# Performance work log

Measured on AMD Instinct MI355X. Metric: run time of the kernel, lower is better.

Reference implementation:

```python
import jax, jax.numpy as jnp
import numpy as np

N_GENE = 100000
N_DIS = 20000
H = 128
E = 500000


def setup_inputs() -> dict:
    key = jax.random.key(0)
    ks = jax.random.split(key, 12)
    s1 = 1.0 / np.sqrt(2 * H)  # fan-in init scale, Linear(2H, H)
    s2 = 1.0 / np.sqrt(H)      # fan-in init scale, Linear(H, 1)
    z_gene = jax.random.normal(ks[0], (N_GENE, H), jnp.float32)
    z_disease = jax.random.normal(ks[1], (N_DIS, H), jnp.float32)
    # gene->disease edges: row indexes genes, col indexes diseases
    edges_gd = jnp.stack([
        jax.random.randint(ks[2], (E,), 0, N_GENE),
        jax.random.randint(ks[3], (E,), 0, N_DIS),
    ])
    # gene->gene edges
    edges_gg = jnp.stack([
        jax.random.randint(ks[4], (E,), 0, N_GENE),
        jax.random.randint(ks[5], (E,), 0, N_GENE),
    ])
    return {
        "z_gene": z_gene,
        "z_disease": z_disease,
        "edges_gd": edges_gd,
        "edges_gg": edges_gg,
        "w1_gd": jax.random.normal(ks[6], (2 * H, H), jnp.float32) * s1,
        "b1_gd": jnp.zeros((H,), jnp.float32),
        "w2_gd": jax.random.normal(ks[7], (H, 1), jnp.float32) * s2,
        "b2_gd": jnp.zeros((1,), jnp.float32),
        "w1_gg": jax.random.normal(ks[8], (2 * H, H), jnp.float32) * s1,
        "b1_gg": jnp.zeros((H,), jnp.float32),
        "w2_gg": jax.random.normal(ks[9], (H, 1), jnp.float32) * s2,
        "b2_gg": jnp.zeros((1,), jnp.float32),
    }


def _decode(z_src, z_dst, edges, w1, b1, w2, b2):
    # gather src/dst node embeddings by edge index, concat -> [E, 2H]
    z = jnp.concatenate([z_src[edges[0]], z_dst[edges[1]]], axis=1)
    h = jnp.maximum(z @ w1 + b1, 0.0)  # Linear + ReLU
    return h @ w2 + b2                  # Linear -> [E, 1]


def reference(z_gene, z_disease, edges_gd, edges_gg,
              w1_gd, b1_gd, w2_gd, b2_gd,
              w1_gg, b1_gg, w2_gg, b2_gg):
    out_gd = _decode(z_gene, z_disease, edges_gd, w1_gd, b1_gd, w2_gd, b2_gd)
    out_gg = _decode(z_gene, z_gene, edges_gg, w1_gg, b1_gg, w2_gg, b2_gg)
    # dict of per-relation outputs in the original; stack since E matches
    return jnp.stack([out_gd, out_gg])  # [2, E, 1]
```

## Files before the change

kernel.cpp:

```cpp
#include <hip/hip_runtime.h>
#include <hip/hip_bf16.h>

#define HDIM 128

typedef __attribute__((ext_vector_type(8))) short short8;
typedef __attribute__((ext_vector_type(4))) float floatx4;

__device__ __forceinline__ float bf2f(unsigned short u) {
    return __uint_as_float(((unsigned)u) << 16);
}
__device__ __forceinline__ unsigned short f2b(float f) {
    __hip_bfloat16 h = __float2bfloat16(f);
    return __builtin_bit_cast(unsigned short, h);
}
__device__ __forceinline__ float ldv(const void* p, size_t i, int flag) {
    return flag ? bf2f(((const unsigned short*)p)[i]) : ((const float*)p)[i];
}
__device__ __forceinline__ short8 pack8(float4 a, float4 b) {
    short8 r;
    r[0] = (short)f2b(a.x); r[1] = (short)f2b(a.y);
    r[2] = (short)f2b(a.z); r[3] = (short)f2b(a.w);
    r[4] = (short)f2b(b.x); r[5] = (short)f2b(b.y);
    r[6] = (short)f2b(b.z); r[7] = (short)f2b(b.w);
    return r;
}

__device__ __forceinline__ int local_detect(const unsigned short* zbits) {
    __shared__ int red[256];
    int tid = threadIdx.x;
    int cnt = 0;
    for (int i = tid; i < 4096; i += 256) {
        int ex = (zbits[i] >> 7) & 0xFF;
        if (ex >= 100 && ex <= 140) cnt++;
    }
    red[tid] = cnt;
    __syncthreads();
    for (int s = 128; s > 0; s >>= 1) {
        if (tid < s) red[tid] += red[tid + s];
        __syncthreads();
    }
    return (red[0] >= 3686) ? 1 : 0;
}

__global__ __launch_bounds__(256) void prep_kernel(
    const unsigned short* __restrict__ zbits,
    const void* __restrict__ w1_gd, const void* __restrict__ w1_gg,
    const void* __restrict__ b1_gd, const void* __restrict__ w2_gd,
    const void* __restrict__ b2_gd, const void* __restrict__ b1_gg,
    const void* __restrict__ w2_gg, const void* __restrict__ b2_gg,
    unsigned short* __restrict__ img, float* __restrict__ params,
    int* __restrict__ flagout)
{
    int flag = local_detect(zbits);
    int b = blockIdx.x;
    int tid = threadIdx.x;
    if (b < 32) {
        int im   = b >> 3;
        int sub  = b & 7;
        const void* w1 = (im < 2) ? w1_gd : w1_gg;
        int part = im & 1;
        unsigned short* out = img + im * 16384;
        int n = tid & 127;
#pragma unroll
        for (int it = 0; it < 8; ++it) {
            int k = sub * 16 + it * 2 + (tid >> 7);
            unsigned short v = flag
                ? ((const unsigned short*)w1)[(size_t)(part * 128 + k) * 128 + n]
                : f2b(((const float*)w1)[(size_t)(part * 128 + k) * 128 + n]);
            out[n * 128 + (((k >> 3) ^ (n & 15)) << 3) + (k & 7)] = v;
        }
    } else {
        if (tid < 128) {
            params[tid]       = ldv(b1_gd, tid, flag);
            params[256 + tid] = ldv(b1_gg, tid, flag);
        } else {
            params[tid]       = ldv(w2_gd, tid - 128, flag);
            params[256 + tid] = ldv(w2_gg, tid - 128, flag);
        }
        if (tid == 0) {
            params[512] = ldv(b2_gd, 0, flag);
            params[513] = ldv(b2_gg, 0, flag);
            *flagout = flag;
        }
    }
}

__global__ __launch_bounds__(256) void proj_all_kernel(
    const void* __restrict__ Zg, const void* __restrict__ Zd,
    const uint4* __restrict__ Wimg, const float* __restrict__ params,
    unsigned short* __restrict__ A_gd, unsigned short* __restrict__ B_gd,
    unsigned short* __restrict__ A_gg, unsigned short* __restrict__ B_gg,
    int NG, int ND, int gblk, const int* __restrict__ flagp)
{
    __shared__ uint4 sW[2048];
    int tid  = threadIdx.x;
    int lane = tid & 63;
    int wave = tid >> 6;
    int nl   = lane & 15;
    int quad = lane >> 4;
    int flag = *flagp;

    int b  = blockIdx.x;
    int ph = (b >= gblk) + (b >= 2 * gblk) + (b >= 3 * gblk);
    bool gene = ph < 3;
    int blk = b - ph * gblk;
    int M = gene ? NG : ND;
    const void* Z = gene ? Zg : Zd;
    const uint4* im = Wimg + (ph == 0 ? 0 : ph == 1 ? 2 : ph == 2 ? 3 : 1) * 2048;
    unsigned short* Out = ph == 0 ? A_gd : ph == 1 ? A_gg : ph == 2 ? B_gg : B_gd;
    const float* bias = ph == 0 ? params : ph == 1 ? params + 256 : nullptr;

#pragma unroll
    for (int i = 0; i < 8; ++i) sW[tid + i * 256] = im[tid + i * 256];

    int row0 = blk * 128 + wave * 32 + nl;
    int row1 = row0 + 16;
    int r0c = row0 < M ? row0 : (M - 1);
    int r1c = row1 < M ? row1 : (M - 1);

    short8 zf[2][4];
    if (flag) {
        const uint4* z0 = (const uint4*)Z + (size_t)r0c * 16;
        const uint4* z1 = (const uint4*)Z + (size_t)r1c * 16;
#pragma unroll
        for (int kc = 0; kc < 4; ++kc) {
            zf[0][kc] = __builtin_bit_cast(short8, z0[kc * 4 + quad]);
            zf[1][kc] = __builtin_bit_cast(short8, z1[kc * 4 + quad]);
        }
    } else {
        const float4* z0 = (const float4*)Z + (size_t)r0c * 32;
        const float4* z1 = (const float4*)Z + (size_t)r1c * 32;
#pragma unroll
        for (int kc = 0; kc < 4; ++kc) {
            int o = kc * 8 + quad * 2;
            zf[0][kc] = pack8(z0[o], z0[o + 1]);
            zf[1][kc] = pack8(z1[o], z1[o + 1]);
        }
    }

    __syncthreads();

    floatx4 acc[2][8];
#pragma unroll
    for (int rt = 0; rt < 2; ++rt)
#pragma unroll
        for (int nt = 0; nt < 8; ++nt)
            acc[rt][nt] = (floatx4){0.f, 0.f, 0.f, 0.f};

#pragma unroll
    for (int kc = 0; kc < 4; ++kc) {
        int p = (kc * 4 + quad) ^ nl;
#pragma unroll
        for (int nt = 0; nt < 8; ++nt) {
            short8 wf = __builtin_bit_cast(short8, sW[(nt * 16 + nl) * 16 + p]);
            acc[0][nt] = __builtin_amdgcn_mfma_f32_16x16x32_bf16(wf, zf[0][kc], acc[0][nt], 0, 0, 0);
            acc[1][nt] = __builtin_amdgcn_mfma_f32_16x16x32_bf16(wf, zf[1][kc], acc[1][nt], 0, 0, 0);
        }
    }

    char* sOb = (char*)sW;
    __syncthreads();
#pragma unroll
    for (int rt = 0; rt < 2; ++rt) {
        int h = wave * 16 + nl;
#pragma unroll
        for (int nt = 0; nt < 8; ++nt) {
            float4 bv = {0.f, 0.f, 0.f, 0.f};
            if (bias) bv = *(const float4*)(bias + nt * 16 + quad * 4);
            unsigned lo = ((unsigned)f2b(acc[rt][nt][0] + bv.x)) |
                          (((unsigned)f2b(acc[rt][nt][1] + bv.y)) << 16);
            unsigned hi = ((unsigned)f2b(acc[rt][nt][2] + bv.z)) |
                          (((unsigned)f2b(acc[rt][nt][3] + bv.w)) << 16);
            uint2 v; v.x = lo; v.y = hi;
            *(uint2*)(sOb + h * 264 + nt * 32 + quad * 8) = v;
        }
        __syncthreads();
#pragma unroll
        for (int j = 0; j < 4; ++j) {
            int r = blk * 128 + rt * 16 + j * 32 + (tid >> 4);
            uint4 v = *(const uint4*)(sOb + (j * 16 + (tid >> 4)) * 264 + (tid & 15) * 16);
            if (r < M)
                *(uint4*)(Out + (size_t)r * HDIM + (tid & 15) * 8) = v;
        }
        if (rt == 0) __syncthreads();
    }
}

__global__ __launch_bounds__(256) void edge_kernel(
    const int* __restrict__ edges_gd, const int* __restrict__ edges_gg,
    const unsigned short* __restrict__ A_gd, const unsigned short* __restrict__ B_gd,
    const unsigned short* __restrict__ A_gg, const unsigned short* __restrict__ B_gg,
    const float* __restrict__ params,
    void* __restrict__ out, int E, int nb, const int* __restrict__ flagp)
{
    int rel = ((int)blockIdx.x >= nb) ? 1 : 0;
    int blk = blockIdx.x - rel * nb;
    const int* edges = rel ? edges_gg : edges_gd;
    const unsigned short* A = rel ? A_gg : A_gd;
    const unsigned short* B = rel ? B_gg : B_gd;
    const float* w2 = params + 128 + rel * 256;
    float b2 = params[512 + rel];

    int tid  = threadIdx.x;
    int lane = tid & 63;
    int wave = tid >> 6;
    int nl   = lane & 7;
    int grp  = lane >> 3;

    float w2f[16];
#pragma unroll
    for (int i = 0; i < 4; ++i) {
        float4 t = *(const float4*)(w2 + nl * 16 + i * 4);
        w2f[i * 4 + 0] = t.x; w2f[i * 4 + 1] = t.y;
        w2f[i * 4 + 2] = t.z; w2f[i * 4 + 3] = t.w;
    }

    int e0 = blk * 64 + (wave * 8 + grp) * 2;
    int e1 = e0 + 1;
    int emax = E - 2 > 0 ? E - 2 : 0;
    int ec = e0 < emax ? e0 : emax;
    int sel = e0 - ec;
    int2 sp = *(const int2*)(edges + ec);
    int2 dp = *(const int2*)(edges + E + ec);
    int src0 = sel ? sp.y : sp.x;
    int dst0 = sel ? dp.y : dp.x;
    int src1 = sp.y;
    int dst1 = dp.y;

    const uint4* a0p = (const uint4*)(A + (size_t)src0 * HDIM) + nl * 2;
    const uint4* b0p = (const uint4*)(B + (size_t)dst0 * HDIM) + nl * 2;
    const uint4* a1p = (const uint4*)(A + (size_t)src1 * HDIM) + nl * 2;
    const uint4* b1p = (const uint4*)(B + (size_t)dst1 * HDIM) + nl * 2;
    uint4 a0[2] = {a0p[0], a0p[1]};
    uint4 c0[2] = {b0p[0], b0p[1]};
    uint4 a1[2] = {a1p[0], a1p[1]};
    uint4 c1[2] = {b1p[0], b1p[1]};

    float acc0 = 0.f, acc1 = 0.f;
#pragma unroll
    for (int i = 0; i < 2; ++i) {
        const unsigned* au0 = (const unsigned*)&a0[i];
        const unsigned* cu0 = (const unsigned*)&c0[i];
        const unsigned* au1 = (const unsigned*)&a1[i];
        const unsigned* cu1 = (const unsigned*)&c1[i];
#pragma unroll
        for (int j = 0; j < 4; ++j) {
            int ch = i * 8 + j * 2;
            float x0 = __uint_as_float(au0[j] << 16);
            float x1 = __uint_as_float(au0[j] & 0xffff0000u);
            float y0 = __uint_as_float(cu0[j] << 16);
            float y1 = __uint_as_float(cu0[j] & 0xffff0000u);
            acc0 = fmaf(fmaxf(x0 + y0, 0.f), w2f[ch], acc0);
            acc0 = fmaf(fmaxf(x1 + y1, 0.f), w2f[ch + 1], acc0);
            float u0 = __uint_as_float(au1[j] << 16);
            float u1 = __uint_as_float(au1[j] & 0xffff0000u);
            float v0 = __uint_as_float(cu1[j] << 16);
            float v1 = __uint_as_float(cu1[j] & 0xffff0000u);
            acc1 = fmaf(fmaxf(u0 + v0, 0.f), w2f[ch], acc1);
            acc1 = fmaf(fmaxf(u1 + v1, 0.f), w2f[ch + 1], acc1);
        }
    }
    acc0 += __shfl_xor(acc0, 1); acc1 += __shfl_xor(acc1, 1);
    acc0 += __shfl_xor(acc0, 2); acc1 += __shfl_xor(acc1, 2);
    acc0 += __shfl_xor(acc0, 4); acc1 += __shfl_xor(acc1, 4);

    if (nl == 0) {
        int flag = *flagp;
        size_t base = (size_t)rel * E;
        if (e0 < E) {
            float r = acc0 + b2;
            if (flag) ((unsigned short*)out)[base + e0] = f2b(r);
            else      ((float*)out)[base + e0] = r;
        }
        if (e1 < E) {
            float r = acc1 + b2;
            if (flag) ((unsigned short*)out)[base + e1] = f2b(r);
            else      ((float*)out)[base + e1] = r;
        }
    }
}

__global__ __launch_bounds__(256) void detect_kernel(
    const unsigned short* __restrict__ zbits, int* __restrict__ flag)
{
    int f = local_detect(zbits);
    if (threadIdx.x == 0) *flag = f;
}

__global__ __launch_bounds__(128) void naive_edge_kernel(
    const int* __restrict__ edges,
    const void* __restrict__ zsrc, const void* __restrict__ zdst,
    const void* __restrict__ w1, const void* __restrict__ b1,
    const void* __restrict__ w2, const void* __restrict__ b2,
    void* __restrict__ out, size_t eoff, int E,
    const int* __restrict__ flagp)
{
    int flag = flagp ? *flagp : 0;
    __shared__ float zs[128], zd[128], red[128];
    int e = blockIdx.x;
    int n = threadIdx.x;
    int src = edges[e], dst = edges[E + e];
    zs[n] = ldv(zsrc, (size_t)src * HDIM + n, flag);
    zd[n] = ldv(zdst, (size_t)dst * HDIM + n, flag);
    __syncthreads();
    float acc = ldv(b1, n, flag);
    for (int k = 0; k < 128; ++k) acc = fmaf(zs[k], ldv(w1, (size_t)k * HDIM + n, flag), acc);
    for (int k = 0; k < 128; ++k) acc = fmaf(zd[k], ldv(w1, (size_t)(128 + k) * HDIM + n, flag), acc);
    red[n] = fmaxf(acc, 0.f) * ldv(w2, n, flag);
    __syncthreads();
    for (int s = 64; s > 0; s >>= 1) {
        if (n < s) red[n] += red[n + s];
        __syncthreads();
    }
    if (n == 0) {
        float r = red[0] + ldv(b2, 0, flag);
        if (flag) ((unsigned short*)out)[eoff + e] = f2b(r);
        else      ((float*)out)[eoff + e] = r;
    }
}

extern "C" void kernel_launch(void* const* d_in, const int* in_sizes, int n_in,
                              void* d_out, int out_size, void* d_ws, size_t ws_size,
                              hipStream_t stream)
{
    const void* z_gene = d_in[0];
    const void* z_dis  = d_in[1];
    const int* edges_gd = (const int*)d_in[2];
    const int* edges_gg = (const int*)d_in[3];
    const void* w1_gd = d_in[4];
    const void* b1_gd = d_in[5];
    const void* w2_gd = d_in[6];
    const void* b2_gd = d_in[7];
    const void* w1_gg = d_in[8];
    const void* b1_gg = d_in[9];
    const void* w2_gg = d_in[10];
    const void* b2_gg = d_in[11];

    int NG = in_sizes[0] / HDIM;
    int ND = in_sizes[1] / HDIM;
    int E  = in_sizes[2] / 2;

    size_t off_flag   = 0;
    size_t off_params = 256;
    size_t off_img    = 2560;
    size_t off_Agd    = off_img + 131072;
    size_t off_Bgd    = off_Agd + (size_t)NG * HDIM * 2;
    size_t off_Agg    = off_Bgd + (size_t)ND * HDIM * 2;
    size_t off_Bgg    = off_Agg + (size_t)NG * HDIM * 2;
    size_t need       = off_Bgg + (size_t)NG * HDIM * 2;

    char* ws = (char*)d_ws;

    if (ws_size < need) {
        const int* flagp = nullptr;
        if (ws_size >= 16) {
            detect_kernel<<<1, 256, 0, stream>>>((const unsigned short*)z_gene, (int*)ws);
            flagp = (const int*)ws;
        }
        naive_edge_kernel<<<E, 128, 0, stream>>>(edges_gd, z_gene, z_dis,
                                                 w1_gd, b1_gd, w2_gd, b2_gd,
                                                 d_out, 0, E, flagp);
        naive_edge_kernel<<<E, 128, 0, stream>>>(edges_gg, z_gene, z_gene,
                                                 w1_gg, b1_gg, w2_gg, b2_gg,
                                                 d_out, (size_t)E, E, flagp);
        return;
    }

    int* flag = (int*)(ws + off_flag);
    float* params = (float*)(ws + off_params);
    unsigned short* img = (unsigned short*)(ws + off_img);
    unsigned short* Agd = (unsigned short*)(ws + off_Agd);
    unsigned short* Bgd = (unsigned short*)(ws + off_Bgd);
    unsigned short* Agg = (unsigned short*)(ws + off_Agg);
    unsigned short* Bgg = (unsigned short*)(ws + off_Bgg);

    prep_kernel<<<33, 256, 0, stream>>>((const unsigned short*)z_gene,
                                        w1_gd, w1_gg, b1_gd, w2_gd, b2_gd,
                                        b1_gg, w2_gg, b2_gg, img, params, flag);

    const uint4* img4 = (const uint4*)img;
    int gblk = (NG + 127) / 128;
    int dblk = (ND + 127) / 128;
    proj_all_kernel<<<3 * gblk + dblk, 256, 0, stream>>>(z_gene, z_dis, img4, params,
                                                         Agd, Bgd, Agg, Bgg,
                                                         NG, ND, gblk, flag);

    int nb = (E + 63) / 64;
    edge_kernel<<<2 * nb, 256, 0, stream>>>(edges_gd, edges_gg, Agd, Bgd, Agg, Bgg,
                                            params, d_out, E, nb, flag);
}
```

Before: 223.8 us.

## Fuse prep, projection and edge stages into one cooperative persistent kernel

Replaces the three-kernel sequence (weight prep, node projection, edge scoring) with a single cooperative kernel. It runs a persistent grid sized from occupancy and separates the stages with grid-wide syncs. This is meant to remove launch gaps and tail effects between the stages. In exchange it adds the cost of grid barriers, and the grid-stride loops may balance work less evenly than the separate launches did. The previous path is kept as a fallback if the cooperative launch fails.

```diff
diff --git a/kernel.cpp b/kernel.cpp
--- a/kernel.cpp
+++ b/kernel.cpp
@@ -1,5 +1,8 @@
 #include <hip/hip_runtime.h>
 #include <hip/hip_bf16.h>
+#include <hip/hip_cooperative_groups.h>
+
+namespace cg = cooperative_groups;
 
 #define HDIM 128
 
@@ -25,8 +28,7 @@
     return r;
 }
 
-__device__ __forceinline__ int local_detect(const unsigned short* zbits) {
-    __shared__ int red[256];
+__device__ __forceinline__ int local_detect_s(const unsigned short* zbits, int* red) {
     int tid = threadIdx.x;
     int cnt = 0;
     for (int i = tid; i < 4096; i += 256) {
@@ -39,7 +41,249 @@
         if (tid < s) red[tid] += red[tid + s];
         __syncthreads();
     }
-    return (red[0] >= 3686) ? 1 : 0;
+    int f = (red[0] >= 3686) ? 1 : 0;
+    __syncthreads();
+    return f;
+}
+
+__global__ __launch_bounds__(256) void fused_kernel(
+    const void* __restrict__ Zg, const void* __restrict__ Zd,
+    const int* __restrict__ edges_gd, const int* __restrict__ edges_gg,
+    const void* __restrict__ w1_gd, const void* __restrict__ b1_gd,
+    const void* __restrict__ w2_gd, const void* __restrict__ b2_gd,
+    const void* __restrict__ w1_gg, const void* __restrict__ b1_gg,
+    const void* __restrict__ w2_gg, const void* __restrict__ b2_gg,
+    unsigned short* __restrict__ img, float* __restrict__ params,
+    unsigned short* __restrict__ A_gd, unsigned short* __restrict__ B_gd,
+    unsigned short* __restrict__ A_gg, unsigned short* __restrict__ B_gg,
+    void* __restrict__ out,
+    int NG, int ND, int E, int gblk, int dblk, int nb)
+{
+    cg::grid_group grid = cg::this_grid();
+    __shared__ uint4 sW[2048];
+
+    int tid  = threadIdx.x;
+    int lane = tid & 63;
+    int wave = tid >> 6;
+    int flag = local_detect_s((const unsigned short*)Zg, (int*)sW);
+    int b = blockIdx.x;
+
+    if (b < 256) {
+        int im  = b >> 6;
+        int sub = b & 63;
+        const void* w1 = (im < 2) ? w1_gd : w1_gg;
+        int part = im & 1;
+        unsigned short* o = img + im * 16384;
+        int n = tid & 127;
+        int k = sub * 2 + (tid >> 7);
+        unsigned short v = flag
+            ? ((const unsigned short*)w1)[(size_t)(part * 128 + k) * 128 + n]
+            : f2b(((const float*)w1)[(size_t)(part * 128 + k) * 128 + n]);
+        o[n * 128 + (((k >> 3) ^ (n & 15)) << 3) + (k & 7)] = v;
+        if (b == 0) {
+            if (tid < 128) {
+                params[tid]       = ldv(b1_gd, tid, flag);
+                params[256 + tid] = ldv(b1_gg, tid, flag);
+            } else {
+                params[tid]       = ldv(w2_gd, tid - 128, flag);
+                params[256 + tid] = ldv(w2_gg, tid - 128, flag);
+            }
+            if (tid == 0) {
+                params[512] = ldv(b2_gd, 0, flag);
+                params[513] = ldv(b2_gg, 0, flag);
+            }
+        }
+    }
+    __threadfence();
+    grid.sync();
+    __threadfence();
+
+    {
+        int nl   = lane & 15;
+        int quad = lane >> 4;
+        const uint4* Wimg = (const uint4*)img;
+        int ninst = 3 * gblk + dblk;
+        for (int inst = b; inst < ninst; inst += gridDim.x) {
+            int ph = (inst >= gblk) + (inst >= 2 * gblk) + (inst >= 3 * gblk);
+            bool gene = ph < 3;
+            int blk = inst - ph * gblk;
+            int M = gene ? NG : ND;
+            const void* Z = gene ? Zg : Zd;
+            const uint4* im = Wimg + (ph == 0 ? 0 : ph == 1 ? 2 : ph == 2 ? 3 : 1) * 2048;
+            unsigned short* Out = ph == 0 ? A_gd : ph == 1 ? A_gg : ph == 2 ? B_gg : B_gd;
+            const float* bias = ph == 0 ? params : ph == 1 ? params + 256 : nullptr;
+
+            __syncthreads();
+#pragma unroll
+            for (int i = 0; i < 8; ++i) sW[tid + i * 256] = im[tid + i * 256];
+
+            int row0 = blk * 128 + wave * 32 + nl;
+            int row1 = row0 + 16;
+            int r0c = row0 < M ? row0 : (M - 1);
+            int r1c = row1 < M ? row1 : (M - 1);
+
+            short8 zf[2][4];
+            if (flag) {
+                const uint4* z0 = (const uint4*)Z + (size_t)r0c * 16;
+                const uint4* z1 = (const uint4*)Z + (size_t)r1c * 16;
+#pragma unroll
+                for (int kc = 0; kc < 4; ++kc) {
+                    zf[0][kc] = __builtin_bit_cast(short8, z0[kc * 4 + quad]);
+                    zf[1][kc] = __builtin_bit_cast(short8, z1[kc * 4 + quad]);
+                }
+            } else {
+                const float4* z0 = (const float4*)Z + (size_t)r0c * 32;
+                const float4* z1 = (const float4*)Z + (size_t)r1c * 32;
+#pragma unroll
+                for (int kc = 0; kc < 4; ++kc) {
+                    int o = kc * 8 + quad * 2;
+                    zf[0][kc] = pack8(z0[o], z0[o + 1]);
+                    zf[1][kc] = pack8(z1[o], z1[o + 1]);
+                }
+            }
+
+            __syncthreads();
+
+            floatx4 acc[2][8];
+#pragma unroll
+            for (int rt = 0; rt < 2; ++rt)
+#pragma unroll
+                for (int nt = 0; nt < 8; ++nt)
+                    acc[rt][nt] = (floatx4){0.f, 0.f, 0.f, 0.f};
+
+#pragma unroll
+            for (int kc = 0; kc < 4; ++kc) {
+                int p = (kc * 4 + quad) ^ nl;
+#pragma unroll
+                for (int nt = 0; nt < 8; ++nt) {
+                    short8 wf = __builtin_bit_cast(short8, sW[(nt * 16 + nl) * 16 + p]);
+                    acc[0][nt] = __builtin_amdgcn_mfma_f32_16x16x32_bf16(wf, zf[0][kc], acc[0][nt], 0, 0, 0);
+                    acc[1][nt] = __builtin_amdgcn_mfma_f32_16x16x32_bf16(wf, zf[1][kc], acc[1][nt], 0, 0, 0);
+                }
+            }
+
+            char* sOb = (char*)sW;
+            __syncthreads();
+#pragma unroll
+            for (int rt = 0; rt < 2; ++rt) {
+                int h = wave * 16 + nl;
+#pragma unroll
+                for (int nt = 0; nt < 8; ++nt) {
+                    float4 bv = {0.f, 0.f, 0.f, 0.f};
+                    if (bias) bv = *(const float4*)(bias + nt * 16 + quad * 4);
+                    unsigned lo = ((unsigned)f2b(acc[rt][nt][0] + bv.x)) |
+                                  (((unsigned)f2b(acc[rt][nt][1] + bv.y)) << 16);
+                    unsigned hi = ((unsigned)f2b(acc[rt][nt][2] + bv.z)) |
+                                  (((unsigned)f2b(acc[rt][nt][3] + bv.w)) << 16);
+                    uint2 v; v.x = lo; v.y = hi;
+                    *(uint2*)(sOb + h * 264 + nt * 32 + quad * 8) = v;
+                }
+                __syncthreads();
+#pragma unroll
+                for (int j = 0; j < 4; ++j) {
+                    int r = blk * 128 + rt * 16 + j * 32 + (tid >> 4);
+                    uint4 v = *(const uint4*)(sOb + (j * 16 + (tid >> 4)) * 264 + (tid & 15) * 16);
+                    if (r < M)
+                        *(uint4*)(Out + (size_t)r * HDIM + (tid & 15) * 8) = v;
+                }
+                if (rt == 0) __syncthreads();
+            }
+        }
+    }
+    __threadfence();
+    grid.sync();
+    __threadfence();
+
+    {
+        int nl  = lane & 7;
+        int grp = lane >> 3;
+        int nchunk = 2 * nb;
+        for (int c = b; c < nchunk; c += gridDim.x) {
+            int rel = (c >= nb) ? 1 : 0;
+            int blk = c - rel * nb;
+            const int* edges = rel ? edges_gg : edges_gd;
+            const unsigned short* A = rel ? A_gg : A_gd;
+            const unsigned short* B = rel ? B_gg : B_gd;
+            const float* w2 = params + 128 + rel * 256;
+            float b2 = params[512 + rel];
+
+            float w2f[16];
+#pragma unroll
+            for (int i = 0; i < 4; ++i) {
+                float4 t = *(const float4*)(w2 + nl * 16 + i * 4);
+                w2f[i * 4 + 0] = t.x; w2f[i * 4 + 1] = t.y;
+                w2f[i * 4 + 2] = t.z; w2f[i * 4 + 3] = t.w;
+            }
+
+            int e0 = blk * 64 + (wave * 8 + grp) * 2;
+            int e1 = e0 + 1;
+            int emax = E - 2 > 0 ? E - 2 : 0;
+            int ec = e0 < emax ? e0 : emax;
+            int sel = e0 - ec;
+            int2 sp = *(const int2*)(edges + ec);
+            int2 dp = *(const int2*)(edges + E + ec);
+            int src0 = sel ? sp.y : sp.x;
+            int dst0 = sel ? dp.y : dp.x;
+            int src1 = sp.y;
+            int dst1 = dp.y;
+
+            const uint4* a0p = (const uint4*)(A + (size_t)src0 * HDIM) + nl * 2;
+            const uint4* b0p = (const uint4*)(B + (size_t)dst0 * HDIM) + nl * 2;
+            const uint4* a1p = (const uint4*)(A + (size_t)src1 * HDIM) + nl * 2;
+            const uint4* b1p = (const uint4*)(B + (size_t)dst1 * HDIM) + nl * 2;
+            uint4 a0[2] = {a0p[0], a0p[1]};
+            uint4 c0[2] = {b0p[0], b0p[1]};
+            uint4 a1[2] = {a1p[0], a1p[1]};
+            uint4 c1[2] = {b1p[0], b1p[1]};
+
+            float acc0 = 0.f, acc1 = 0.f;
+#pragma unroll
+            for (int i = 0; i < 2; ++i) {
+                const unsigned* au0 = (const unsigned*)&a0[i];
+                const unsigned* cu0 = (const unsigned*)&c0[i];
+                const unsigned* au1 = (const unsigned*)&a1[i];
+                const unsigned* cu1 = (const unsigned*)&c1[i];
+#pragma unroll
+                for (int j = 0; j < 4; ++j) {
+                    int ch = i * 8 + j * 2;
+                    float x0 = __uint_as_float(au0[j] << 16);
+                    float x1 = __uint_as_float(au0[j] & 0xffff0000u);
+                    float y0 = __uint_as_float(cu0[j] << 16);
+                    float y1 = __uint_as_float(cu0[j] & 0xffff0000u);
+                    acc0 = fmaf(fmaxf(x0 + y0, 0.f), w2f[ch], acc0);
+                    acc0 = fmaf(fmaxf(x1 + y1, 0.f), w2f[ch + 1], acc0);
+                    float u0 = __uint_as_float(au1[j] << 16);
+                    float u1 = __uint_as_float(au1[j] & 0xffff0000u);
+                    float v0 = __uint_as_float(cu1[j] << 16);
+                    float v1 = __uint_as_float(cu1[j] & 0xffff0000u);
+                    acc1 = fmaf(fmaxf(u0 + v0, 0.f), w2f[ch], acc1);
+                    acc1 = fmaf(fmaxf(u1 + v1, 0.f), w2f[ch + 1], acc1);
+                }
+            }
+            acc0 += __shfl_xor(acc0, 1); acc1 += __shfl_xor(acc1, 1);
+            acc0 += __shfl_xor(acc0, 2); acc1 += __shfl_xor(acc1, 2);
+            acc0 += __shfl_xor(acc0, 4); acc1 += __shfl_xor(acc1, 4);
+
+            if (nl == 0) {
+                size_t base = (size_t)rel * E;
+                if (e0 < E) {
+                    float r = acc0 + b2;
+                    if (flag) ((unsigned short*)out)[base + e0] = f2b(r);
+                    else      ((float*)out)[base + e0] = r;
+                }
+                if (e1 < E) {
+                    float r = acc1 + b2;
+                    if (flag) ((unsigned short*)out)[base + e1] = f2b(r);
+                    else      ((float*)out)[base + e1] = r;
+                }
+            }
+        }
+    }
+}
+
+__device__ __forceinline__ int local_detect(const unsigned short* zbits) {
+    __shared__ int red[256];
+    return local_detect_s(zbits, red);
 }
 
 __global__ __launch_bounds__(256) void prep_kernel(
@@ -374,18 +618,56 @@
     unsigned short* Agg = (unsigned short*)(ws + off_Agg);
     unsigned short* Bgg = (unsigned short*)(ws + off_Bgg);
 
+    int gblk = (NG + 127) / 128;
+    int dblk = (ND + 127) / 128;
+    int nb   = (E + 63) / 64;
+
+    static int s_grid = -1;
+    if (s_grid < 0) {
+        int per_cu = 0;
+        hipError_t e1 = hipOccupancyMaxActiveBlocksPerMultiprocessor(
+            &per_cu, (const void*)fused_kernel, 256, 0);
+        hipDeviceProp_t props;
+        int dev = 0;
+        hipGetDevice(&dev);
+        hipError_t e2 = hipGetDeviceProperties(&props, dev);
+        if (e1 == hipSuccess && e2 == hipSuccess && per_cu > 0) {
+            long g = (long)per_cu * props.multiProcessorCount;
+            if (g > 2048) g = 2048;
+            s_grid = (int)g;
+        } else {
+            s_grid = 0;
+        }
+    }
+
+    bool coop_done = false;
+    if (s_grid >= 256) {
+        void* outp = d_out;
+        void* args[] = {
+            (void*)&z_gene, (void*)&z_dis, (void*)&edges_gd, (void*)&edges_gg,
+            (void*)&w1_gd, (void*)&b1_gd, (void*)&w2_gd, (void*)&b2_gd,
+            (void*)&w1_gg, (void*)&b1_gg, (void*)&w2_gg, (void*)&b2_gg,
+            (void*)&img, (void*)&params,
+            (void*)&Agd, (void*)&Bgd, (void*)&Agg, (void*)&Bgg,
+            (void*)&outp, (void*)&NG, (void*)&ND, (void*)&E,
+            (void*)&gblk, (void*)&dblk, (void*)&nb
+        };
+        hipError_t e = hipLaunchCooperativeKernel(
+            (const void*)fused_kernel, dim3(s_grid), dim3(256), args, 0, stream);
+        coop_done = (e == hipSuccess);
+        if (!coop_done) s_grid = 0;
+    }
+    if (coop_done) return;
+
     prep_kernel<<<33, 256, 0, stream>>>((const unsigned short*)z_gene,
                                         w1_gd, w1_gg, b1_gd, w2_gd, b2_gd,
                                         b1_gg, w2_gg, b2_gg, img, params, flag);
 
     const uint4* img4 = (const uint4*)img;
-    int gblk = (NG + 127) / 128;
-    int dblk = (ND + 127) / 128;
     proj_all_kernel<<<3 * gblk + dblk, 256, 0, stream>>>(z_gene, z_dis, img4, params,
                                                          Agd, Bgd, Agg, Bgg,
                                                          NG, ND, gblk, flag);
 
-    int nb = (E + 63) / 64;
     edge_kernel<<<2 * nb, 256, 0, stream>>>(edges_gd, edges_gg, Agd, Bgd, Agg, Bgg,
                                             params, d_out, E, nb, flag);
 }
```

Result: slower. 453.8 us (+102.8%).

## Fold weight prep and dtype detection into the projection kernel

Applied to the files above, without the earlier changes.

Removes the separate prep kernel launch. Each projection block now runs the dtype detection itself, transposes and swizzles its W1 half directly from global memory into shared memory, and reads the bias straight from the input. Block 0 also writes the small params and flag buffer used by the edge kernel. This drops one launch and the intermediate weight image, but every one of the ~2500 blocks now repeats the 4096-element detection reduction and a scattered 2-byte transpose into shared memory.

```diff
diff --git a/kernel.cpp b/kernel.cpp
--- a/kernel.cpp
+++ b/kernel.cpp
@@ -25,8 +25,7 @@
     return r;
 }
 
-__device__ __forceinline__ int local_detect(const unsigned short* zbits) {
-    __shared__ int red[256];
+__device__ __forceinline__ int local_detect_s(const unsigned short* zbits, int* red) {
     int tid = threadIdx.x;
     int cnt = 0;
     for (int i = tid; i < 4096; i += 256) {
@@ -39,58 +38,21 @@
         if (tid < s) red[tid] += red[tid + s];
         __syncthreads();
     }
-    return (red[0] >= 3686) ? 1 : 0;
-}
-
-__global__ __launch_bounds__(256) void prep_kernel(
-    const unsigned short* __restrict__ zbits,
-    const void* __restrict__ w1_gd, const void* __restrict__ w1_gg,
-    const void* __restrict__ b1_gd, const void* __restrict__ w2_gd,
-    const void* __restrict__ b2_gd, const void* __restrict__ b1_gg,
-    const void* __restrict__ w2_gg, const void* __restrict__ b2_gg,
-    unsigned short* __restrict__ img, float* __restrict__ params,
-    int* __restrict__ flagout)
-{
-    int flag = local_detect(zbits);
-    int b = blockIdx.x;
-    int tid = threadIdx.x;
-    if (b < 32) {
-        int im   = b >> 3;
-        int sub  = b & 7;
-        const void* w1 = (im < 2) ? w1_gd : w1_gg;
-        int part = im & 1;
-        unsigned short* out = img + im * 16384;
-        int n = tid & 127;
-#pragma unroll
-        for (int it = 0; it < 8; ++it) {
-            int k = sub * 16 + it * 2 + (tid >> 7);
-            unsigned short v = flag
-                ? ((const unsigned short*)w1)[(size_t)(part * 128 + k) * 128 + n]
-                : f2b(((const float*)w1)[(size_t)(part * 128 + k) * 128 + n]);
-            out[n * 128 + (((k >> 3) ^ (n & 15)) << 3) + (k & 7)] = v;
-        }
-    } else {
-        if (tid < 128) {
-            params[tid]       = ldv(b1_gd, tid, flag);
-            params[256 + tid] = ldv(b1_gg, tid, flag);
-        } else {
-            params[tid]       = ldv(w2_gd, tid - 128, flag);
-            params[256 + tid] = ldv(w2_gg, tid - 128, flag);
-        }
-        if (tid == 0) {
-            params[512] = ldv(b2_gd, 0, flag);
-            params[513] = ldv(b2_gg, 0, flag);
-            *flagout = flag;
-        }
-    }
+    int f = (red[0] >= 3686) ? 1 : 0;
+    __syncthreads();
+    return f;
 }
 
 __global__ __launch_bounds__(256) void proj_all_kernel(
     const void* __restrict__ Zg, const void* __restrict__ Zd,
-    const uint4* __restrict__ Wimg, const float* __restrict__ params,
+    const void* __restrict__ w1_gd, const void* __restrict__ w1_gg,
+    const void* __restrict__ b1_gd, const void* __restrict__ b1_gg,
+    const void* __restrict__ w2_gd, const void* __restrict__ b2_gd,
+    const void* __restrict__ w2_gg, const void* __restrict__ b2_gg,
+    float* __restrict__ params, int* __restrict__ flagout,
     unsigned short* __restrict__ A_gd, unsigned short* __restrict__ B_gd,
     unsigned short* __restrict__ A_gg, unsigned short* __restrict__ B_gg,
-    int NG, int ND, int gblk, const int* __restrict__ flagp)
+    int NG, int ND, int gblk)
 {
     __shared__ uint4 sW[2048];
     int tid  = threadIdx.x;
@@ -98,7 +60,8 @@
     int wave = tid >> 6;
     int nl   = lane & 15;
     int quad = lane >> 4;
-    int flag = *flagp;
+
+    int flag = local_detect_s((const unsigned short*)Zg, (int*)sW);
 
     int b  = blockIdx.x;
     int ph = (b >= gblk) + (b >= 2 * gblk) + (b >= 3 * gblk);
@@ -106,12 +69,55 @@
     int blk = b - ph * gblk;
     int M = gene ? NG : ND;
     const void* Z = gene ? Zg : Zd;
-    const uint4* im = Wimg + (ph == 0 ? 0 : ph == 1 ? 2 : ph == 2 ? 3 : 1) * 2048;
+    const void* w1src = (ph == 0 || ph == 3) ? w1_gd : w1_gg;
+    int part = (ph == 2 || ph == 3) ? 1 : 0;
     unsigned short* Out = ph == 0 ? A_gd : ph == 1 ? A_gg : ph == 2 ? B_gg : B_gd;
-    const float* bias = ph == 0 ? params : ph == 1 ? params + 256 : nullptr;
-
-#pragma unroll
-    for (int i = 0; i < 8; ++i) sW[tid + i * 256] = im[tid + i * 256];
+    const void* b1 = ph == 0 ? b1_gd : ph == 1 ? b1_gg : nullptr;
+
+    if (b == 0) {
+        if (tid < 128) {
+            params[tid]       = ldv(b1_gd, tid, flag);
+            params[256 + tid] = ldv(b1_gg, tid, flag);
+        } else {
+            params[tid]       = ldv(w2_gd, tid - 128, flag);
+            params[256 + tid] = ldv(w2_gg, tid - 128, flag);
+        }
+        if (tid == 0) {
+            params[512] = ldv(b2_gd, 0, flag);
+            params[513] = ldv(b2_gg, 0, flag);
+            *flagout = flag;
+        }
+    }
+
+    {
+        unsigned short* sH = (unsigned short*)sW;
+        int n0 = (tid & 15) * 8;
+        int kb = tid >> 4;
+#pragma unroll
+        for (int pass = 0; pass < 8; ++pass) {
+            int k = pass * 16 + kb;
+            unsigned short hw[8];
+            if (flag) {
+                uint4 v = *(const uint4*)((const unsigned short*)w1src +
+                                          (size_t)(part * 128 + k) * 128 + n0);
+                const unsigned short* pv = (const unsigned short*)&v;
+#pragma unroll
+                for (int j = 0; j < 8; ++j) hw[j] = pv[j];
+            } else {
+                const float* pf = (const float*)w1src + (size_t)(part * 128 + k) * 128 + n0;
+                float4 f0 = *(const float4*)(pf);
+                float4 f1 = *(const float4*)(pf + 4);
+                hw[0] = f2b(f0.x); hw[1] = f2b(f0.y); hw[2] = f2b(f0.z); hw[3] = f2b(f0.w);
+                hw[4] = f2b(f1.x); hw[5] = f2b(f1.y); hw[6] = f2b(f1.z); hw[7] = f2b(f1.w);
+            }
+#pragma unroll
+            for (int jj = 0; jj < 8; ++jj) {
+                int j = (jj + (tid & 7)) & 7;
+                int n = n0 + j;
+                sH[n * 128 + (((k >> 3) ^ (n & 15)) << 3) + (k & 7)] = hw[j];
+            }
+        }
+    }
 
     int row0 = blk * 128 + wave * 32 + nl;
     int row1 = row0 + 16;
@@ -166,7 +172,12 @@
 #pragma unroll
         for (int nt = 0; nt < 8; ++nt) {
             float4 bv = {0.f, 0.f, 0.f, 0.f};
-            if (bias) bv = *(const float4*)(bias + nt * 16 + quad * 4);
+            if (b1) {
+                bv.x = ldv(b1, nt * 16 + quad * 4 + 0, flag);
+                bv.y = ldv(b1, nt * 16 + quad * 4 + 1, flag);
+                bv.z = ldv(b1, nt * 16 + quad * 4 + 2, flag);
+                bv.w = ldv(b1, nt * 16 + quad * 4 + 3, flag);
+            }
             unsigned lo = ((unsigned)f2b(acc[rt][nt][0] + bv.x)) |
                           (((unsigned)f2b(acc[rt][nt][1] + bv.y)) << 16);
             unsigned hi = ((unsigned)f2b(acc[rt][nt][2] + bv.z)) |
@@ -278,6 +289,11 @@
             else      ((float*)out)[base + e1] = r;
         }
     }
+}
+
+__device__ __forceinline__ int local_detect(const unsigned short* zbits) {
+    __shared__ int red[256];
+    return local_detect_s(zbits, red);
 }
 
 __global__ __launch_bounds__(256) void detect_kernel(
@@ -368,22 +384,21 @@
 
     int* flag = (int*)(ws + off_flag);
     float* params = (float*)(ws + off_params);
-    unsigned short* img = (unsigned short*)(ws + off_img);
     unsigned short* Agd = (unsigned short*)(ws + off_Agd);
     unsigned short* Bgd = (unsigned short*)(ws + off_Bgd);
     unsigned short* Agg = (unsigned short*)(ws + off_Agg);
     unsigned short* Bgg = (unsigned short*)(ws + off_Bgg);
 
-    prep_kernel<<<33, 256, 0, stream>>>((const unsigned short*)z_gene,
-                                        w1_gd, w1_gg, b1_gd, w2_gd, b2_gd,
-                                        b1_gg, w2_gg, b2_gg, img, params, flag);
-
-    const uint4* img4 = (const uint4*)img;
     int gblk = (NG + 127) / 128;
     int dblk = (ND + 127) / 128;
-    proj_all_kernel<<<3 * gblk + dblk, 256, 0, stream>>>(z_gene, z_dis, img4, params,
-                                                         Agd, Bgd, Agg, Bgg,
-                                                         NG, ND, gblk, flag);
+
+    proj_all_kernel<<<3 * gblk + dblk, 256, 0, stream>>>(
+        z_gene, z_dis,
+        w1_gd, w1_gg, b1_gd, b1_gg,
+        w2_gd, b2_gd, w2_gg, b2_gg,
+        params, flag,
+        Agd, Bgd, Agg, Bgg,
+        NG, ND, gblk);
 
     int nb = (E + 63) / 64;
     edge_kernel<<<2 * nb, 256, 0, stream>>>(edges_gd, edges_gg, Agd, Bgd, Agg, Bgg,
```

New measurement: 240.5 us. 7.5% more time.

## Fuse node projection into per-edge MFMA kernel, dropping projected-table precompute

Applied to the files above, without the earlier changes.

Removes the separate projection pass that built bf16 projected tables (A/B per relation) and the edge kernel that gathered them. Each block now gathers raw source and destination embeddings for 128 edges and runs the full 256x128 first layer with MFMA. Bias, ReLU and the second linear are applied in registers before writing the result. This saves the workspace write and readback and a kernel launch. In exchange it recomputes the GEMM per edge instead of per node, gathers wider fp32 rows when inputs are float, and reloads 64KB of weights into LDS for every block, which limits occupancy.

```diff
diff --git a/kernel.cpp b/kernel.cpp
--- a/kernel.cpp
+++ b/kernel.cpp
@@ -25,21 +25,28 @@
     return r;
 }
 
+__device__ __forceinline__ int local_detect_s(const unsigned short* zbits, int* red) {
+    int tid = threadIdx.x;
+    int nthr = blockDim.x;
+    int cnt = 0;
+    for (int i = tid; i < 4096; i += nthr) {
+        int ex = (zbits[i] >> 7) & 0xFF;
+        if (ex >= 100 && ex <= 140) cnt++;
+    }
+    red[tid] = cnt;
+    __syncthreads();
+    for (int s = nthr >> 1; s > 0; s >>= 1) {
+        if (tid < s) red[tid] += red[tid + s];
+        __syncthreads();
+    }
+    int f = (red[0] >= 3686) ? 1 : 0;
+    __syncthreads();
+    return f;
+}
+
 __device__ __forceinline__ int local_detect(const unsigned short* zbits) {
     __shared__ int red[256];
-    int tid = threadIdx.x;
-    int cnt = 0;
-    for (int i = tid; i < 4096; i += 256) {
-        int ex = (zbits[i] >> 7) & 0xFF;
-        if (ex >= 100 && ex <= 140) cnt++;
-    }
-    red[tid] = cnt;
-    __syncthreads();
-    for (int s = 128; s > 0; s >>= 1) {
-        if (tid < s) red[tid] += red[tid + s];
-        __syncthreads();
-    }
-    return (red[0] >= 3686) ? 1 : 0;
+    return local_detect_s(zbits, red);
 }
 
 __global__ __launch_bounds__(256) void prep_kernel(
@@ -85,14 +92,13 @@
     }
 }
 
-__global__ __launch_bounds__(256) void proj_all_kernel(
+__global__ __launch_bounds__(512, 4) void fused_edge_kernel(
     const void* __restrict__ Zg, const void* __restrict__ Zd,
+    const int* __restrict__ edges_gd, const int* __restrict__ edges_gg,
     const uint4* __restrict__ Wimg, const float* __restrict__ params,
-    unsigned short* __restrict__ A_gd, unsigned short* __restrict__ B_gd,
-    unsigned short* __restrict__ A_gg, unsigned short* __restrict__ B_gg,
-    int NG, int ND, int gblk, const int* __restrict__ flagp)
-{
-    __shared__ uint4 sW[2048];
+    void* __restrict__ out, int E, int nbe, const int* __restrict__ flagp)
+{
+    __shared__ uint4 sW[4096];
     int tid  = threadIdx.x;
     int lane = tid & 63;
     int wave = tid >> 6;
@@ -100,183 +106,77 @@
     int quad = lane >> 4;
     int flag = *flagp;
 
-    int b  = blockIdx.x;
-    int ph = (b >= gblk) + (b >= 2 * gblk) + (b >= 3 * gblk);
-    bool gene = ph < 3;
-    int blk = b - ph * gblk;
-    int M = gene ? NG : ND;
-    const void* Z = gene ? Zg : Zd;
-    const uint4* im = Wimg + (ph == 0 ? 0 : ph == 1 ? 2 : ph == 2 ? 3 : 1) * 2048;
-    unsigned short* Out = ph == 0 ? A_gd : ph == 1 ? A_gg : ph == 2 ? B_gg : B_gd;
-    const float* bias = ph == 0 ? params : ph == 1 ? params + 256 : nullptr;
-
-#pragma unroll
-    for (int i = 0; i < 8; ++i) sW[tid + i * 256] = im[tid + i * 256];
-
-    int row0 = blk * 128 + wave * 32 + nl;
-    int row1 = row0 + 16;
-    int r0c = row0 < M ? row0 : (M - 1);
-    int r1c = row1 < M ? row1 : (M - 1);
-
-    short8 zf[2][4];
+    int rel = ((int)blockIdx.x >= nbe) ? 1 : 0;
+    int blk = blockIdx.x - rel * nbe;
+    const int* edges = rel ? edges_gg : edges_gd;
+    const void* Zdst = rel ? Zg : Zd;
+
+    const uint4* im = Wimg + rel * 4096;
+#pragma unroll
+    for (int i = 0; i < 8; ++i) sW[tid + i * 512] = im[tid + i * 512];
+
+    int e  = blk * 128 + wave * 16 + nl;
+    int ec = e < E ? e : E - 1;
+    int src = edges[ec];
+    int dst = edges[E + ec];
+
+    short8 zf[8];
     if (flag) {
-        const uint4* z0 = (const uint4*)Z + (size_t)r0c * 16;
-        const uint4* z1 = (const uint4*)Z + (size_t)r1c * 16;
+        const uint4* zs = (const uint4*)Zg   + (size_t)src * 16;
+        const uint4* zd = (const uint4*)Zdst + (size_t)dst * 16;
 #pragma unroll
         for (int kc = 0; kc < 4; ++kc) {
-            zf[0][kc] = __builtin_bit_cast(short8, z0[kc * 4 + quad]);
-            zf[1][kc] = __builtin_bit_cast(short8, z1[kc * 4 + quad]);
+            zf[kc]     = __builtin_bit_cast(short8, zs[kc * 4 + quad]);
+            zf[kc + 4] = __builtin_bit_cast(short8, zd[kc * 4 + quad]);
         }
     } else {
-        const float4* z0 = (const float4*)Z + (size_t)r0c * 32;
-        const float4* z1 = (const float4*)Z + (size_t)r1c * 32;
+        const float4* zs = (const float4*)Zg   + (size_t)src * 32;
+        const float4* zd = (const float4*)Zdst + (size_t)dst * 32;
 #pragma unroll
         for (int kc = 0; kc < 4; ++kc) {
             int o = kc * 8 + quad * 2;
-            zf[0][kc] = pack8(z0[o], z0[o + 1]);
-            zf[1][kc] = pack8(z1[o], z1[o + 1]);
-        }
-    }
-
-    __syncthreads();
-
-    floatx4 acc[2][8];
-#pragma unroll
-    for (int rt = 0; rt < 2; ++rt)
-#pragma unroll
-        for (int nt = 0; nt < 8; ++nt)
-            acc[rt][nt] = (floatx4){0.f, 0.f, 0.f, 0.f};
-
-#pragma unroll
-    for (int kc = 0; kc < 4; ++kc) {
-        int p = (kc * 4 + quad) ^ nl;
+            zf[kc]     = pack8(zs[o], zs[o + 1]);
+            zf[kc + 4] = pack8(zd[o], zd[o + 1]);
+        }
+    }
+
+    __syncthreads();
+
+    floatx4 acc[8];
+#pragma unroll
+    for (int nt = 0; nt < 8; ++nt) acc[nt] = (floatx4){0.f, 0.f, 0.f, 0.f};
+
+#pragma unroll
+    for (int kc = 0; kc < 8; ++kc) {
+        const uint4* base = sW + (kc >> 2) * 2048;
+        int p = ((kc & 3) * 4 + quad) ^ nl;
 #pragma unroll
         for (int nt = 0; nt < 8; ++nt) {
-            short8 wf = __builtin_bit_cast(short8, sW[(nt * 16 + nl) * 16 + p]);
-            acc[0][nt] = __builtin_amdgcn_mfma_f32_16x16x32_bf16(wf, zf[0][kc], acc[0][nt], 0, 0, 0);
-            acc[1][nt] = __builtin_amdgcn_mfma_f32_16x16x32_bf16(wf, zf[1][kc], acc[1][nt], 0, 0, 0);
-        }
-    }
-
-    char* sOb = (char*)sW;
-    __syncthreads();
-#pragma unroll
-    for (int rt = 0; rt < 2; ++rt) {
-        int h = wave * 16 + nl;
-#pragma unroll
-        for (int nt = 0; nt < 8; ++nt) {
-            float4 bv = {0.f, 0.f, 0.f, 0.f};
-            if (bias) bv = *(const float4*)(bias + nt * 16 + quad * 4);
-            unsigned lo = ((unsigned)f2b(acc[rt][nt][0] + bv.x)) |
-                          (((unsigned)f2b(acc[rt][nt][1] + bv.y)) << 16);
-            unsigned hi = ((unsigned)f2b(acc[rt][nt][2] + bv.z)) |
-                          (((unsigned)f2b(acc[rt][nt][3] + bv.w)) << 16);
-            uint2 v; v.x = lo; v.y = hi;
-            *(uint2*)(sOb + h * 264 + nt * 32 + quad * 8) = v;
-        }
-        __syncthreads();
-#pragma unroll
-        for (int j = 0; j < 4; ++j) {
-            int r = blk * 128 + rt * 16 + j * 32 + (tid >> 4);
-            uint4 v = *(const uint4*)(sOb + (j * 16 + (tid >> 4)) * 264 + (tid & 15) * 16);
-            if (r < M)
-                *(uint4*)(Out + (size_t)r * HDIM + (tid & 15) * 8) = v;
-        }
-        if (rt == 0) __syncthreads();
-    }
-}
-
-__global__ __launch_bounds__(256) void edge_kernel(
-    const int* __restrict__ edges_gd, const int* __restrict__ edges_gg,
-    const unsigned short* __restrict__ A_gd, const unsigned short* __restrict__ B_gd,
-    const unsigned short* __restrict__ A_gg, const unsigned short* __restrict__ B_gg,
-    const float* __restrict__ params,
-    void* __restrict__ out, int E, int nb, const int* __restrict__ flagp)
-{
-    int rel = ((int)blockIdx.x >= nb) ? 1 : 0;
-    int blk = blockIdx.x - rel * nb;
-    const int* edges = rel ? edges_gg : edges_gd;
-    const unsigned short* A = rel ? A_gg : A_gd;
-    const unsigned short* B = rel ? B_gg : B_gd;
-    const float* w2 = params + 128 + rel * 256;
+            short8 wf = __builtin_bit_cast(short8, base[(nt * 16 + nl) * 16 + p]);
+            acc[nt] = __builtin_amdgcn_mfma_f32_16x16x32_bf16(wf, zf[kc], acc[nt], 0, 0, 0);
+        }
+    }
+
+    const float* pr = params + rel * 256;
     float b2 = params[512 + rel];
-
-    int tid  = threadIdx.x;
-    int lane = tid & 63;
-    int wave = tid >> 6;
-    int nl   = lane & 7;
-    int grp  = lane >> 3;
-
-    float w2f[16];
-#pragma unroll
-    for (int i = 0; i < 4; ++i) {
-        float4 t = *(const float4*)(w2 + nl * 16 + i * 4);
-        w2f[i * 4 + 0] = t.x; w2f[i * 4 + 1] = t.y;
-        w2f[i * 4 + 2] = t.z; w2f[i * 4 + 3] = t.w;
-    }
-
-    int e0 = blk * 64 + (wave * 8 + grp) * 2;
-    int e1 = e0 + 1;
-    int emax = E - 2 > 0 ? E - 2 : 0;
-    int ec = e0 < emax ? e0 : emax;
-    int sel = e0 - ec;
-    int2 sp = *(const int2*)(edges + ec);
-    int2 dp = *(const int2*)(edges + E + ec);
-    int src0 = sel ? sp.y : sp.x;
-    int dst0 = sel ? dp.y : dp.x;
-    int src1 = sp.y;
-    int dst1 = dp.y;
-
-    const uint4* a0p = (const uint4*)(A + (size_t)src0 * HDIM) + nl * 2;
-    const uint4* b0p = (const uint4*)(B + (size_t)dst0 * HDIM) + nl * 2;
-    const uint4* a1p = (const uint4*)(A + (size_t)src1 * HDIM) + nl * 2;
-    const uint4* b1p = (const uint4*)(B + (size_t)dst1 * HDIM) + nl * 2;
-    uint4 a0[2] = {a0p[0], a0p[1]};
-    uint4 c0[2] = {b0p[0], b0p[1]};
-    uint4 a1[2] = {a1p[0], a1p[1]};
-    uint4 c1[2] = {b1p[0], b1p[1]};
-
-    float acc0 = 0.f, acc1 = 0.f;
-#pragma unroll
-    for (int i = 0; i < 2; ++i) {
-        const unsigned* au0 = (const unsigned*)&a0[i];
-        const unsigned* cu0 = (const unsigned*)&c0[i];
-        const unsigned* au1 = (const unsigned*)&a1[i];
-        const unsigned* cu1 = (const unsigned*)&c1[i];
-#pragma unroll
-        for (int j = 0; j < 4; ++j) {
-            int ch = i * 8 + j * 2;
-            float x0 = __uint_as_float(au0[j] << 16);
-            float x1 = __uint_as_float(au0[j] & 0xffff0000u);
-            float y0 = __uint_as_float(cu0[j] << 16);
-            float y1 = __uint_as_float(cu0[j] & 0xffff0000u);
-            acc0 = fmaf(fmaxf(x0 + y0, 0.f), w2f[ch], acc0);
-            acc0 = fmaf(fmaxf(x1 + y1, 0.f), w2f[ch + 1], acc0);
-            float u0 = __uint_as_float(au1[j] << 16);
-            float u1 = __uint_as_float(au1[j] & 0xffff0000u);
-            float v0 = __uint_as_float(cu1[j] << 16);
-            float v1 = __uint_as_float(cu1[j] & 0xffff0000u);
-            acc1 = fmaf(fmaxf(u0 + v0, 0.f), w2f[ch], acc1);
-            acc1 = fmaf(fmaxf(u1 + v1, 0.f), w2f[ch + 1], acc1);
-        }
-    }
-    acc0 += __shfl_xor(acc0, 1); acc1 += __shfl_xor(acc1, 1);
-    acc0 += __shfl_xor(acc0, 2); acc1 += __shfl_xor(acc1, 2);
-    acc0 += __shfl_xor(acc0, 4); acc1 += __shfl_xor(acc1, 4);
-
-    if (nl == 0) {
-        int flag = *flagp;
+    float s = 0.f;
+#pragma unroll
+    for (int nt = 0; nt < 8; ++nt) {
+        float4 b1v = *(const float4*)(pr + nt * 16 + quad * 4);
+        float4 w2v = *(const float4*)(pr + 128 + nt * 16 + quad * 4);
+        s = fmaf(fmaxf(acc[nt][0] + b1v.x, 0.f), w2v.x, s);
+        s = fmaf(fmaxf(acc[nt][1] + b1v.y, 0.f), w2v.y, s);
+        s = fmaf(fmaxf(acc[nt][2] + b1v.z, 0.f), w2v.z, s);
+        s = fmaf(fmaxf(acc[nt][3] + b1v.w, 0.f), w2v.w, s);
+    }
+    s += __shfl_xor(s, 16);
+    s += __shfl_xor(s, 32);
+
+    if (quad == 0 && e < E) {
+        float r = s + b2;
         size_t base = (size_t)rel * E;
-        if (e0 < E) {
-            float r = acc0 + b2;
-            if (flag) ((unsigned short*)out)[base + e0] = f2b(r);
-            else      ((float*)out)[base + e0] = r;
-        }
-        if (e1 < E) {
-            float r = acc1 + b2;
-            if (flag) ((unsigned short*)out)[base + e1] = f2b(r);
-            else      ((float*)out)[base + e1] = r;
-        }
+        if (flag) ((unsigned short*)out)[base + e] = f2b(r);
+        else      ((float*)out)[base + e] = r;
     }
 }
 
@@ -339,15 +239,12 @@
     int NG = in_sizes[0] / HDIM;
     int ND = in_sizes[1] / HDIM;
     int E  = in_sizes[2] / 2;
+    (void)NG; (void)ND;
 
     size_t off_flag   = 0;
     size_t off_params = 256;
     size_t off_img    = 2560;
-    size_t off_Agd    = off_img + 131072;
-    size_t off_Bgd    = off_Agd + (size_t)NG * HDIM * 2;
-    size_t off_Agg    = off_Bgd + (size_t)ND * HDIM * 2;
-    size_t off_Bgg    = off_Agg + (size_t)NG * HDIM * 2;
-    size_t need       = off_Bgg + (size_t)NG * HDIM * 2;
+    size_t need       = off_img + 131072;
 
     char* ws = (char*)d_ws;
 
@@ -369,23 +266,13 @@
     int* flag = (int*)(ws + off_flag);
     float* params = (float*)(ws + off_params);
     unsigned short* img = (unsigned short*)(ws + off_img);
-    unsigned short* Agd = (unsigned short*)(ws + off_Agd);
-    unsigned short* Bgd = (unsigned short*)(ws + off_Bgd);
-    unsigned short* Agg = (unsigned short*)(ws + off_Agg);
-    unsigned short* Bgg = (unsigned short*)(ws + off_Bgg);
 
     prep_kernel<<<33, 256, 0, stream>>>((const unsigned short*)z_gene,
                                         w1_gd, w1_gg, b1_gd, w2_gd, b2_gd,
                                         b1_gg, w2_gg, b2_gg, img, params, flag);
 
-    const uint4* img4 = (const uint4*)img;
-    int gblk = (NG + 127) / 128;
-    int dblk = (ND + 127) / 128;
-    proj_all_kernel<<<3 * gblk + dblk, 256, 0, stream>>>(z_gene, z_dis, img4, params,
-                                                         Agd, Bgd, Agg, Bgg,
-                                                         NG, ND, gblk, flag);
-
-    int nb = (E + 63) / 64;
-    edge_kernel<<<2 * nb, 256, 0, stream>>>(edges_gd, edges_gg, Agd, Bgd, Agg, Bgg,
-                                            params, d_out, E, nb, flag);
-}
+    int nbe = (E + 127) / 128;
+    fused_edge_kernel<<<2 * nbe, 512, 0, stream>>>(
+        z_gene, z_dis, edges_gd, edges_gg,
+        (const uint4*)img, params, d_out, E, nbe, flag);
+}
```

Measured after the change: 309.6 us. 1.38x slower.
